# Optimization experiments

Measured on AMD Instinct MI355X. Metric: run time of the kernel, lower is better.

The kernel has to match this reference:

```python
import jax, jax.numpy as jnp
import numpy as np

N, E, F_IN, H = 50000, 800000, 500, 96

def setup_inputs() -> dict:
    key = jax.random.key(0)
    ks = jax.random.split(key, 10)
    x = jax.random.normal(ks[0], (N, F_IN), dtype=jnp.float32)
    src = jax.random.randint(ks[1], (E,), 0, N, dtype=jnp.int32)
    dst = jax.random.randint(ks[2], (E,), 0, N, dtype=jnp.int32)
    perm = jax.random.permutation(ks[3], N).astype(jnp.int32)
    W1 = jax.random.normal(ks[4], (F_IN, H), dtype=jnp.float32) / np.sqrt(F_IN)
    b1 = jnp.zeros((H,), jnp.float32)
    a1 = jnp.full((H,), 0.25, jnp.float32)  # PReLU init
    W2 = jax.random.normal(ks[5], (H, H), dtype=jnp.float32) / np.sqrt(H)
    b2 = jnp.zeros((H,), jnp.float32)
    a2 = jnp.full((H,), 0.25, jnp.float32)
    Wm = jax.random.normal(ks[6], (H, H), dtype=jnp.float32) / np.sqrt(H)
    bm = jnp.zeros((H,), jnp.float32)
    return {"x": x, "src": src, "dst": dst, "perm": perm,
            "W1": W1, "b1": b1, "a1": a1, "W2": W2, "b2": b2, "a2": a2,
            "Wm": Wm, "bm": bm}

def reference(x, src, dst, perm, W1, b1, a1, W2, b2, a2, Wm, bm):
    n = x.shape[0]
    ones = jnp.ones_like(src, dtype=x.dtype)
    deg_out = jnp.clip(jax.ops.segment_sum(ones, src, num_segments=n), 1.0)
    deg_in = jnp.clip(jax.ops.segment_sum(ones, dst, num_segments=n), 1.0)
    norm_out = (deg_out ** -0.5)[:, None]  # [N,1]
    norm_in = (deg_in ** -0.5)[:, None]

    def gconv(h, W, b, a):
        # DGL GraphConv, norm='both': D_out^-1/2 -> W -> A -> D_in^-1/2 -> +b -> PReLU
        h = (h * norm_out) @ W                                  # [N,H]
        agg = jax.ops.segment_sum(h[src], dst, num_segments=n)  # SpMM via gather/scatter
        h = agg * norm_in + b
        return jnp.where(h >= 0, h, a * h)                      # PReLU

    def encode(feat):
        h = gconv(feat, W1, b1, a1)
        return gconv(h, W2, b2, a2)

    z1 = encode(x)
    z2 = encode(x[perm])  # corrupted view: permuted node features
    z1 = z1 @ Wm + bm
    z2 = z2 @ Wm + bm
    return jnp.concatenate([z1.sum(1), z2.sum(1)], axis=0)  # [2N]
```

## Files before the change

kernel.cpp:

```cpp
#include <hip/hip_runtime.h>

#define H96 96

typedef __attribute__((ext_vector_type(8))) short bf16x8_t;
typedef __attribute__((ext_vector_type(4))) float f32x4_t;
typedef __attribute__((ext_vector_type(8))) _Float16 half8_t;

#define NRANGE 8
#define NCHUNK 64

__global__ __launch_bounds__(256) void hist2_kernel(const int* __restrict__ src,
                                                    const int* __restrict__ dst,
                                                    unsigned short* __restrict__ parts,
                                                    int E, int RS, int ecpc) {
    extern __shared__ int h[];
    int r = blockIdx.x >> 6;
    int c = blockIdx.x & 63;
    int lo = r * RS;
    for (int i = threadIdx.x; i < 2 * RS; i += 256) h[i] = 0;
    __syncthreads();
    int e0 = c * ecpc;
    int e1 = min(e0 + ecpc, E);
    for (int base = e0 + threadIdx.x * 4; base < e1; base += 1024) {
        int cnt = min(4, e1 - base);
        if (cnt == 4) {
            int4 sv = *(const int4*)(src + base);
            int4 dv = *(const int4*)(dst + base);
            int a;
            a = sv.x - lo; if ((unsigned)a < (unsigned)RS) atomicAdd(&h[a], 1);
            a = sv.y - lo; if ((unsigned)a < (unsigned)RS) atomicAdd(&h[a], 1);
            a = sv.z - lo; if ((unsigned)a < (unsigned)RS) atomicAdd(&h[a], 1);
            a = sv.w - lo; if ((unsigned)a < (unsigned)RS) atomicAdd(&h[a], 1);
            a = dv.x - lo; if ((unsigned)a < (unsigned)RS) atomicAdd(&h[RS + a], 1);
            a = dv.y - lo; if ((unsigned)a < (unsigned)RS) atomicAdd(&h[RS + a], 1);
            a = dv.z - lo; if ((unsigned)a < (unsigned)RS) atomicAdd(&h[RS + a], 1);
            a = dv.w - lo; if ((unsigned)a < (unsigned)RS) atomicAdd(&h[RS + a], 1);
        } else {
            for (int k = 0; k < cnt; k++) {
                int a = src[base + k] - lo;
                if ((unsigned)a < (unsigned)RS) atomicAdd(&h[a], 1);
                a = dst[base + k] - lo;
                if ((unsigned)a < (unsigned)RS) atomicAdd(&h[RS + a], 1);
            }
        }
    }
    __syncthreads();
    unsigned short* po = parts + ((size_t)(r * 2 + 0) * NCHUNK + c) * RS;
    unsigned short* pi = parts + ((size_t)(r * 2 + 1) * NCHUNK + c) * RS;
    for (int i = threadIdx.x; i < RS; i += 256) {
        po[i] = (unsigned short)h[i];
        pi[i] = (unsigned short)h[RS + i];
    }
}

__global__ void degred_kernel(const unsigned short* __restrict__ parts,
                              const int* __restrict__ perm,
                              int* __restrict__ deg_in, int* __restrict__ iperm,
                              float* __restrict__ no, float* __restrict__ ni,
                              int N, int RS) {
    int i = blockIdx.x * 256 + threadIdx.x;
    if (i >= N) return;
    int r = i / RS, idx = i - r * RS;
    const unsigned short* po = parts + ((size_t)(r * 2 + 0) * NCHUNK) * RS + idx;
    const unsigned short* pi = parts + ((size_t)(r * 2 + 1) * NCHUNK) * RS + idx;
    int so = 0, si = 0;
#pragma unroll
    for (int c = 0; c < NCHUNK; c++) {
        so += po[(size_t)c * RS];
        si += pi[(size_t)c * RS];
    }
    deg_in[i] = si;
    no[i] = rsqrtf(fmaxf((float)so, 1.0f));
    ni[i] = rsqrtf(fmaxf((float)si, 1.0f));
    iperm[perm[i]] = i;
}

__global__ void chunkpre_kernel(const unsigned short* __restrict__ parts,
                                const int* __restrict__ row_start,
                                int* __restrict__ cpre, int N, int RS) {
    int i = blockIdx.x * 256 + threadIdx.x;
    if (i >= N) return;
    int r = i / RS, idx = i - r * RS;
    const unsigned short* pi = parts + ((size_t)(r * 2 + 1) * NCHUNK) * RS + idx;
    int run = row_start[i];
#pragma unroll
    for (int c = 0; c < NCHUNK; c++) {
        cpre[(size_t)c * N + i] = run;
        run += pi[(size_t)c * RS];
    }
}

__global__ void scanA_kernel(const int* __restrict__ in, int* __restrict__ pre,
                             int* __restrict__ bsums, int n) {
    __shared__ int s[256];
    int i = blockIdx.x * 256 + threadIdx.x;
    int v = (i < n) ? in[i] : 0;
    s[threadIdx.x] = v;
    __syncthreads();
    for (int off = 1; off < 256; off <<= 1) {
        int t = (threadIdx.x >= off) ? s[threadIdx.x - off] : 0;
        __syncthreads();
        s[threadIdx.x] += t;
        __syncthreads();
    }
    if (i < n) pre[i] = s[threadIdx.x] - v;
    if (threadIdx.x == 255) bsums[blockIdx.x] = s[255];
}

__global__ void scanB_kernel(int* __restrict__ bsums, int nb) {
    __shared__ int s[256];
    int v = (threadIdx.x < nb) ? bsums[threadIdx.x] : 0;
    s[threadIdx.x] = v;
    __syncthreads();
    for (int off = 1; off < 256; off <<= 1) {
        int t = (threadIdx.x >= off) ? s[threadIdx.x - off] : 0;
        __syncthreads();
        s[threadIdx.x] += t;
        __syncthreads();
    }
    if (threadIdx.x < nb) bsums[threadIdx.x] = s[threadIdx.x] - v;
}

__global__ void rowfin_kernel(const int* __restrict__ pre, const int* __restrict__ bsums,
                              int* __restrict__ row_start, int N, int E) {
    int i = blockIdx.x * 256 + threadIdx.x;
    if (i < N) row_start[i] = pre[i] + bsums[blockIdx.x];
    if (i == 0) row_start[N] = E;
}

__global__ __launch_bounds__(256) void scatter8_kernel(const int* __restrict__ src,
                                                       const int* __restrict__ dst,
                                                       const float* __restrict__ norm_out,
                                                       const int* __restrict__ cpre,
                                                       int2* __restrict__ edge2,
                                                       int E, int N, int RS, int ecpc) {
    extern __shared__ int cur[];
    int r = blockIdx.x >> 6, c = blockIdx.x & 63;
    int lo = r * RS;
    int len = min(RS, N - lo);
    for (int i = threadIdx.x; i < len; i += 256)
        cur[i] = cpre[(size_t)c * N + lo + i];
    __syncthreads();
    int e0 = c * ecpc, e1 = min(e0 + ecpc, E);
    for (int e = e0 + threadIdx.x; e < e1; e += 256) {
        int d = dst[e] - lo;
        if ((unsigned)d < (unsigned)len) {
            int s = src[e];
            int p = atomicAdd(&cur[d], 1);
            edge2[p] = make_int2(s, __float_as_int(norm_out[s]));
        }
    }
}

__global__ void histblk_kernel(const int* __restrict__ deg, int* __restrict__ hb,
                               int N, int nb) {
    __shared__ int h[256];
    h[threadIdx.x] = 0;
    __syncthreads();
    int i = blockIdx.x * 256 + threadIdx.x;
    if (i < N) atomicAdd(&h[min(deg[i], 255)], 1);
    __syncthreads();
    hb[threadIdx.x * nb + blockIdx.x] = h[threadIdx.x];
}

__global__ void place2_kernel(const int* __restrict__ deg, const int* __restrict__ hpre,
                              const int* __restrict__ bsums, int* __restrict__ order,
                              int N, int nb) {
    __shared__ int cur[256];
    int idx = threadIdx.x * nb + blockIdx.x;
    cur[threadIdx.x] = hpre[idx] + bsums[idx >> 8];
    __syncthreads();
    int i = blockIdx.x * 256 + threadIdx.x;
    if (i < N) {
        int b = min(deg[i], 255);
        int p = atomicAdd(&cur[b], 1);
        order[p] = i;
    }
}

__device__ __forceinline__ void f2bf2(float v, unsigned short& h, unsigned short& l) {
    unsigned int b = __float_as_uint(v);
    unsigned short hh = (unsigned short)((b + 0x7FFFu + ((b >> 16) & 1u)) >> 16);
    float fh = __uint_as_float(((unsigned int)hh) << 16);
    float r = v - fh;
    unsigned int rb = __float_as_uint(r);
    unsigned short ll = (unsigned short)((rb + 0x7FFFu + ((rb >> 16) & 1u)) >> 16);
    h = hh; l = ll;
}

__device__ __forceinline__ void cvt8(const float f[8], bf16x8_t& ah, bf16x8_t& al) {
    union { unsigned int u[4]; bf16x8_t v; } H, L;
#pragma unroll
    for (int i = 0; i < 4; i++) {
        float v0 = f[2 * i], v1 = f[2 * i + 1];
        unsigned int b0 = __float_as_uint(v0);
        unsigned int b1 = __float_as_uint(v1);
        unsigned int m0 = b0 & 0xFFFF0000u;
        unsigned int m1 = b1 & 0xFFFF0000u;
        float r0 = v0 - __uint_as_float(m0);
        float r1 = v1 - __uint_as_float(m1);
        H.u[i] = (b0 >> 16) | m1;
        L.u[i] = (__float_as_uint(r0) >> 16) | (__float_as_uint(r1) & 0xFFFF0000u);
    }
    ah = H.v; al = L.v;
}

__global__ void weights_prep(const float* __restrict__ W1, const float* __restrict__ W2,
                             const float* __restrict__ Wm, const float* __restrict__ bm,
                             unsigned short* __restrict__ w1h, unsigned short* __restrict__ w1l,
                             unsigned short* __restrict__ w2h, unsigned short* __restrict__ w2l,
                             float* __restrict__ wsum, float* __restrict__ bsum,
                             int F, int KP1) {
    int idx = blockIdx.x * 256 + threadIdx.x;
    int z1 = 96 * KP1, z2 = z1 + 96 * 96;
    if (idx < z1) {
        int n = idx / KP1, k = idx - n * KP1;
        float v = (k < F) ? W1[(size_t)k * 96 + n] : 0.f;
        unsigned short h, l;
        f2bf2(v, h, l);
        w1h[idx] = h; w1l[idx] = l;
    } else if (idx < z2) {
        int t = idx - z1;
        int n = t / 96, k = t - n * 96;
        float v = W2[(size_t)k * 96 + n];
        unsigned short h, l;
        f2bf2(v, h, l);
        w2h[t] = h; w2l[t] = l;
    } else if (idx < z2 + 96) {
        int c = idx - z2;
        float s = 0.f;
        for (int j = 0; j < 96; j++) s += Wm[c * 96 + j];
        wsum[c] = s;
    } else if (idx == z2 + 96) {
        float s = 0.f;
        for (int j = 0; j < 96; j++) s += bm[j];
        bsum[0] = s;
    }
}

#define GBK 32

__device__ __forceinline__ void gload_lds16(const void* g, void* l) {
    __builtin_amdgcn_global_load_lds(
        (const __attribute__((address_space(1))) unsigned int*)g,
        (__attribute__((address_space(3))) unsigned int*)l, 16, 0, 0);
}

__global__ __launch_bounds__(256, 6) void gemm_mfma(const void* __restrict__ Av,
                                                    const unsigned short* __restrict__ Bth,
                                                    const unsigned short* __restrict__ Btl,
                                                    _Float16* __restrict__ C16,
                                                    const int* __restrict__ ipermArr,
                                                    int M, int K, int KP) {
    __shared__ alignas(16) unsigned short Bs[2][2][96][4][8];
    int tid = threadIdx.x;
    int wid = tid >> 6, lane = tid & 63;
    int q = lane >> 4, mn = lane & 15;
    int rg = wid >> 1, ch = wid & 1;
    int row0 = blockIdx.x * 32 + rg * 16;
    int arow = min(row0 + mn, M - 1);
    int nk = (K + GBK - 1) / GBK;

    const float* A32 = (const float*)Av;

    const unsigned short* gsrc[3];
    int lbase[3];
#pragma unroll
    for (int i = 0; i < 3; i++) {
        int c = wid * 192 + i * 64 + lane;
        int part = (c >= 384) ? 1 : 0;
        int rem = c - part * 384;
        int row = rem >> 2, slot = rem & 3;
        int kc = slot ^ ((row >> 1) & 3);
        gsrc[i] = (part ? Btl : Bth) + (size_t)row * KP + kc * 8;
        lbase[i] = (wid * 192 + i * 64) * 8;
    }

    auto stage = [&](int t, int buf) {
#pragma unroll
        for (int i = 0; i < 3; i++)
            gload_lds16(gsrc[i] + (size_t)t * GBK, &Bs[buf][0][0][0][0] + lbase[i]);
    };

    auto loadA = [&](int t, float* f) {
        int gk = t * GBK + q * 8;
        if (gk + 8 <= K) {
            float4 v0 = *(const float4*)(A32 + (size_t)arow * K + gk);
            float4 v1 = *(const float4*)(A32 + (size_t)arow * K + gk + 4);
            f[0] = v0.x; f[1] = v0.y; f[2] = v0.z; f[3] = v0.w;
            f[4] = v1.x; f[5] = v1.y; f[6] = v1.z; f[7] = v1.w;
        } else {
#pragma unroll
            for (int c = 0; c < 8; c++)
                f[c] = (gk + c < K) ? A32[(size_t)arow * K + gk + c] : 0.f;
        }
    };

    f32x4_t acc[3] = {};
    float f[8], fn[8];

    stage(0, 0);
    loadA(0, f);

    int slotR = q ^ ((mn >> 1) & 3);

    for (int t = 0; t < nk; t++) {
        int tn = (t + 1 < nk) ? t + 1 : nk - 1;
        stage(tn, (t + 1) & 1);
        loadA(tn, fn);
        asm volatile("s_waitcnt vmcnt(5)" ::: "memory");
        __builtin_amdgcn_sched_barrier(0);
        __builtin_amdgcn_s_barrier();

        bf16x8_t ah, al;
        cvt8(f, ah, al);

        const unsigned short* bp = &Bs[t & 1][0][0][0][0] + mn * 32 + slotR * 8 + ch * 1536;
#pragma unroll
        for (int ct2 = 0; ct2 < 3; ct2++) {
            bf16x8_t bh = *(const bf16x8_t*)(bp + ct2 * 512);
            bf16x8_t bl = *(const bf16x8_t*)(bp + 3072 + ct2 * 512);
            acc[ct2] = __builtin_amdgcn_mfma_f32_16x16x32_bf16(ah, bh, acc[ct2], 0, 0, 0);
            acc[ct2] = __builtin_amdgcn_mfma_f32_16x16x32_bf16(ah, bl, acc[ct2], 0, 0, 0);
            acc[ct2] = __builtin_amdgcn_mfma_f32_16x16x32_bf16(al, bh, acc[ct2], 0, 0, 0);
        }
        asm volatile("s_waitcnt lgkmcnt(0)" ::: "memory");
        __builtin_amdgcn_sched_barrier(0);
        __builtin_amdgcn_s_barrier();

#pragma unroll
        for (int c = 0; c < 8; c++) f[c] = fn[c];
    }

    asm volatile("s_waitcnt vmcnt(0)" ::: "memory");
    __builtin_amdgcn_sched_barrier(0);

#pragma unroll
    for (int reg = 0; reg < 4; reg++) {
        int gr = row0 + q * 4 + reg;
        if (gr < M) {
            int ip = ipermArr[gr];
#pragma unroll
            for (int ct2 = 0; ct2 < 3; ct2++) {
                int col = (ch * 3 + ct2) * 16 + mn;
                _Float16 v = (_Float16)acc[ct2][reg];
                C16[(size_t)gr * 192 + col] = v;
                C16[(size_t)ip * 192 + 96 + col] = v;
            }
        }
    }
}

__global__ __launch_bounds__(256, 4) void gemm_small(const _Float16* __restrict__ A16,
                                                     const unsigned short* __restrict__ Bth,
                                                     const unsigned short* __restrict__ Btl,
                                                     _Float16* __restrict__ C16,
                                                     int M) {
    __shared__ alignas(16) unsigned short Bs[3][2][96][4][8];
    const int K = 96;
    int tid = threadIdx.x;
    int wid = tid >> 6, lane = tid & 63;
    int q = lane >> 4, mn = lane & 15;
    int row0 = blockIdx.x * 64 + wid * 16;
    int arow = min(row0 + mn, M - 1);

    const unsigned short* gsrc[3];
    int lbase[3];
#pragma unroll
    for (int i = 0; i < 3; i++) {
        int c = wid * 192 + i * 64 + lane;
        int part = (c >= 384) ? 1 : 0;
        int rem = c - part * 384;
        int row = rem >> 2, slot = rem & 3;
        int kc = slot ^ ((row >> 1) & 3);
        gsrc[i] = (part ? Btl : Bth) + (size_t)row * K + kc * 8;
        lbase[i] = (wid * 192 + i * 64) * 8;
    }

#pragma unroll
    for (int t = 0; t < 3; t++)
#pragma unroll
        for (int i = 0; i < 3; i++)
            gload_lds16(gsrc[i] + (size_t)t * GBK, &Bs[t][0][0][0][0] + lbase[i]);

    uint4 ra0 = *(const uint4*)(A16 + (size_t)arow * K + 0 * GBK + q * 8);
    uint4 ra1 = *(const uint4*)(A16 + (size_t)arow * K + 1 * GBK + q * 8);
    uint4 ra2 = *(const uint4*)(A16 + (size_t)arow * K + 2 * GBK + q * 8);

    asm volatile("s_waitcnt vmcnt(0)" ::: "memory");
    __builtin_amdgcn_sched_barrier(0);
    __builtin_amdgcn_s_barrier();

    f32x4_t acc[6] = {};
    int slotR = q ^ ((mn >> 1) & 3);

    auto step = [&](int t, const uint4& raw) {
        float f[8];
        const _Float16* hp = (const _Float16*)&raw;
#pragma unroll
        for (int c = 0; c < 8; c++) f[c] = (float)hp[c];
        bf16x8_t ah, al;
        cvt8(f, ah, al);
        const unsigned short* bp = &Bs[t][0][0][0][0] + mn * 32 + slotR * 8;
#pragma unroll
        for (int ct = 0; ct < 6; ct++) {
            bf16x8_t bh = *(const bf16x8_t*)(bp + ct * 512);
            bf16x8_t bl = *(const bf16x8_t*)(bp + 3072 + ct * 512);
            acc[ct] = __builtin_amdgcn_mfma_f32_16x16x32_bf16(ah, bh, acc[ct], 0, 0, 0);
            acc[ct] = __builtin_amdgcn_mfma_f32_16x16x32_bf16(ah, bl, acc[ct], 0, 0, 0);
            acc[ct] = __builtin_amdgcn_mfma_f32_16x16x32_bf16(al, bh, acc[ct], 0, 0, 0);
        }
    };

    step(0, ra0);
    step(1, ra1);
    step(2, ra2);

#pragma unroll
    for (int reg = 0; reg < 4; reg++) {
        int gr = row0 + q * 4 + reg;
        if (gr < M) {
#pragma unroll
            for (int ct = 0; ct < 6; ct++)
                C16[(size_t)gr * H96 + ct * 16 + mn] = (_Float16)acc[ct][reg];
        }
    }
}

__device__ __forceinline__ void fmah8(float4& a, float4& b, float s, half8_t v) {
    a.x = fmaf(s, (float)v[0], a.x); a.y = fmaf(s, (float)v[1], a.y);
    a.z = fmaf(s, (float)v[2], a.z); a.w = fmaf(s, (float)v[3], a.w);
    b.x = fmaf(s, (float)v[4], b.x); b.y = fmaf(s, (float)v[5], b.y);
    b.z = fmaf(s, (float)v[6], b.z); b.w = fmaf(s, (float)v[7], b.w);
}

__device__ __forceinline__ float4 prelu4(float4 acc, float ni, float4 b, float4 a) {
    float4 h;
    h.x = fmaf(acc.x, ni, b.x); h.x = (h.x >= 0.f) ? h.x : a.x * h.x;
    h.y = fmaf(acc.y, ni, b.y); h.y = (h.y >= 0.f) ? h.y : a.y * h.y;
    h.z = fmaf(acc.z, ni, b.z); h.z = (h.z >= 0.f) ? h.z : a.z * h.z;
    h.w = fmaf(acc.w, ni, b.w); h.w = (h.w >= 0.f) ? h.w : a.w * h.w;
    return h;
}

__global__ __launch_bounds__(384) void spmm1_dual(
        const half8_t* __restrict__ yp, const int* __restrict__ row_start,
        const int2* __restrict__ edge2, const int* __restrict__ order,
        const float* __restrict__ norm_out, const float* __restrict__ norm_in,
        const float* __restrict__ b1, const float* __restrict__ a1,
        half8_t* __restrict__ hpair, int N) {
    int g = blockIdx.x * 32 + threadIdx.y;
    if (g >= N) return;
    int d = order[g];
    int tx = threadIdx.x;
    int beg = row_start[d], end = row_start[d + 1];
    const half8_t* yt = yp + tx;
    float4 a1a = {0,0,0,0}, a1b = {0,0,0,0}, a2a = {0,0,0,0}, a2b = {0,0,0,0};
    int j = beg;
    for (; j + 8 <= end; j += 8) {
        int2 e[8];
#pragma unroll
        for (int q = 0; q < 8; q++) e[q] = edge2[j + q];
        half8_t u[8], w[8];
#pragma unroll
        for (int q = 0; q < 8; q++) u[q] = yt[(size_t)e[q].x * 24];
#pragma unroll
        for (int q = 0; q < 8; q++) w[q] = yt[(size_t)e[q].x * 24 + 12];
#pragma unroll
        for (int q = 0; q < 8; q++) {
            float n = __int_as_float(e[q].y);
            fmah8(a1a, a1b, n, u[q]);
            fmah8(a2a, a2b, n, w[q]);
        }
    }
    for (; j < end; j++) {
        int2 e = edge2[j];
        float n = __int_as_float(e.y);
        fmah8(a1a, a1b, n, yt[(size_t)e.x * 24]);
        fmah8(a2a, a2b, n, yt[(size_t)e.x * 24 + 12]);
    }
    float ni = norm_in[d], no = norm_out[d];
    float4 bb0 = ((const float4*)b1)[tx * 2], bb1 = ((const float4*)b1)[tx * 2 + 1];
    float4 aa0 = ((const float4*)a1)[tx * 2], aa1 = ((const float4*)a1)[tx * 2 + 1];
    float4 r1a = prelu4(a1a, ni, bb0, aa0), r1b = prelu4(a1b, ni, bb1, aa1);
    float4 r2a = prelu4(a2a, ni, bb0, aa0), r2b = prelu4(a2b, ni, bb1, aa1);
    half8_t o1, o2;
    o1[0] = (_Float16)(r1a.x * no); o1[1] = (_Float16)(r1a.y * no);
    o1[2] = (_Float16)(r1a.z * no); o1[3] = (_Float16)(r1a.w * no);
    o1[4] = (_Float16)(r1b.x * no); o1[5] = (_Float16)(r1b.y * no);
    o1[6] = (_Float16)(r1b.z * no); o1[7] = (_Float16)(r1b.w * no);
    o2[0] = (_Float16)(r2a.x * no); o2[1] = (_Float16)(r2a.y * no);
    o2[2] = (_Float16)(r2a.z * no); o2[3] = (_Float16)(r2a.w * no);
    o2[4] = (_Float16)(r2b.x * no); o2[5] = (_Float16)(r2b.y * no);
    o2[6] = (_Float16)(r2b.z * no); o2[7] = (_Float16)(r2b.w * no);
    hpair[(size_t)d * 24 + tx] = o1;
    hpair[(size_t)d * 24 + 12 + tx] = o2;
}

__global__ __launch_bounds__(384) void spmm2_dual(
        const half8_t* __restrict__ th,
        const int* __restrict__ row_start, const int2* __restrict__ edge2,
        const int* __restrict__ order, const float* __restrict__ norm_in,
        const float* __restrict__ b2, const float* __restrict__ a2,
        const float* __restrict__ wsum, const float* __restrict__ bsum,
        float* __restrict__ outp, int N) {
    int g = blockIdx.x * 32 + threadIdx.y;
    int tx = threadIdx.x;
    int ty = threadIdx.y;
    bool valid = (g < N);
    int d = valid ? order[g] : 0;
    int beg = 0, end = 0;
    if (valid) { beg = row_start[d]; end = row_start[d + 1]; }
    const half8_t* t1 = th + tx;
    float4 a1a = {0,0,0,0}, a1b = {0,0,0,0}, a2a = {0,0,0,0}, a2b = {0,0,0,0};
    int j = beg;
    for (; j + 8 <= end; j += 8) {
        int s[8];
#pragma unroll
        for (int q = 0; q < 8; q++) s[q] = edge2[j + q].x;
        half8_t u[8], w[8];
#pragma unroll
        for (int q = 0; q < 8; q++) u[q] = t1[(size_t)s[q] * 24];
#pragma unroll
        for (int q = 0; q < 8; q++) w[q] = t1[(size_t)s[q] * 24 + 12];
#pragma unroll
        for (int q = 0; q < 8; q++) {
            fmah8(a1a, a1b, 1.f, u[q]);
            fmah8(a2a, a2b, 1.f, w[q]);
        }
    }
    for (; j < end; j++) {
        int s = edge2[j].x;
        fmah8(a1a, a1b, 1.f, t1[(size_t)s * 24]);
        fmah8(a2a, a2b, 1.f, t1[(size_t)s * 24 + 12]);
    }
    float ni = valid ? norm_in[d] : 0.f;
    float4 bb0 = ((const float4*)b2)[tx * 2], bb1 = ((const float4*)b2)[tx * 2 + 1];
    float4 aa0 = ((const float4*)a2)[tx * 2], aa1 = ((const float4*)a2)[tx * 2 + 1];
    float4 wv0 = ((const float4*)wsum)[tx * 2], wv1 = ((const float4*)wsum)[tx * 2 + 1];
    float4 r1a = prelu4(a1a, ni, bb0, aa0), r1b = prelu4(a1b, ni, bb1, aa1);
    float4 r2a = prelu4(a2a, ni, bb0, aa0), r2b = prelu4(a2b, ni, bb1, aa1);
    float p1 = r1a.x * wv0.x + r1a.y * wv0.y + r1a.z * wv0.z + r1a.w * wv0.w
             + r1b.x * wv1.x + r1b.y * wv1.y + r1b.z * wv1.z + r1b.w * wv1.w;
    float p2 = r2a.x * wv0.x + r2a.y * wv0.y + r2a.z * wv0.z + r2a.w * wv0.w
             + r2b.x * wv1.x + r2b.y * wv1.y + r2b.z * wv1.z + r2b.w * wv1.w;
    __shared__ float red1[32][12];
    __shared__ float red2[32][12];
    red1[ty][tx] = p1;
    red2[ty][tx] = p2;
    __syncthreads();
    if (tx == 0 && valid) {
        float s1 = 0.f, s2 = 0.f;
#pragma unroll
        for (int k = 0; k < 12; k++) { s1 += red1[ty][k]; s2 += red2[ty][k]; }
        outp[d] = s1 + bsum[0];
        outp[N + d] = s2 + bsum[0];
    }
}

extern "C" void kernel_launch(void* const* d_in, const int* in_sizes, int n_in,
                              void* d_out, int out_size, void* d_ws, size_t ws_size,
                              hipStream_t stream) {
    const float* x    = (const float*)d_in[0];
    const int*   src  = (const int*)d_in[1];
    const int*   dst  = (const int*)d_in[2];
    const int*   perm = (const int*)d_in[3];
    const float* W1   = (const float*)d_in[4];
    const float* b1   = (const float*)d_in[5];
    const float* a1   = (const float*)d_in[6];
    const float* W2   = (const float*)d_in[7];
    const float* b2   = (const float*)d_in[8];
    const float* a2   = (const float*)d_in[9];
    const float* Wm   = (const float*)d_in[10];
    const float* bm   = (const float*)d_in[11];
    float* out = (float*)d_out;

    int E = in_sizes[1];
    int N = in_sizes[3];
    int F = in_sizes[0] / N;
    int KP1 = ((F + GBK - 1) / GBK) * GBK;

    size_t NP = ((size_t)N + 256) & ~(size_t)255;
    size_t EP = ((size_t)E + 255) & ~(size_t)255;
    int nb = (N + 255) / 256;
    size_t HB = ((size_t)256 * nb + 255) & ~(size_t)255;

    int* iperm     = (int*)d_ws;
    int* deg_in    = iperm + NP;
    int* pre       = deg_in + NP;
    int* row_start = pre + NP;
    int* cursor    = row_start + NP;
    int* order     = cursor + NP;
    int* bsums     = order + NP;
    int* hb        = bsums + 256;
    int* hpre      = hb + HB;
    int2* edge2    = (int2*)(hpre + HB);
    float* norm_out = (float*)(edge2 + EP);
    float* norm_in  = norm_out + NP;
    float* wsum     = norm_in + NP;
    float* bsum     = wsum + 128;
    unsigned short* w1th = (unsigned short*)(bsum + 128);
    unsigned short* w1tl = w1th + 49664;
    unsigned short* w2th = w1tl + 49664;
    unsigned short* w2tl = w2th + 9728;
    _Float16* fpA = (_Float16*)(w2tl + 9728);
    _Float16* fpB = fpA + ((size_t)N * 192 + 256);
    _Float16* ypair = fpA;
    _Float16* hpair = fpB;
    _Float16* th    = fpA;

    unsigned short* parts = (unsigned short*)fpA;
    int* cpre = (int*)fpB;

    int RS = (N + NRANGE - 1) / NRANGE;
    int ecpc = ((E + NCHUNK - 1) / NCHUNK + 3) & ~3;
    hist2_kernel<<<NRANGE * NCHUNK, 256, 2 * RS * (int)sizeof(int), stream>>>(
        src, dst, parts, E, RS, ecpc);
    degred_kernel<<<(N + 255) / 256, 256, 0, stream>>>(parts, perm, deg_in, iperm,
                                                       norm_out, norm_in, N, RS);

    scanA_kernel<<<nb, 256, 0, stream>>>(deg_in, pre, bsums, N);
    scanB_kernel<<<1, 256, 0, stream>>>(bsums, nb);
    rowfin_kernel<<<nb, 256, 0, stream>>>(pre, bsums, row_start, N, E);
    chunkpre_kernel<<<(N + 255) / 256, 256, 0, stream>>>(parts, row_start, cpre, N, RS);
    scatter8_kernel<<<NRANGE * NCHUNK, 256, RS * (int)sizeof(int), stream>>>(
        src, dst, norm_out, cpre, edge2, E, N, RS, ecpc);

    histblk_kernel<<<nb, 256, 0, stream>>>(deg_in, hb, N, nb);
    int n2 = 256 * nb;
    int nb2 = (n2 + 255) / 256;
    scanA_kernel<<<nb2, 256, 0, stream>>>(hb, hpre, bsums, n2);
    scanB_kernel<<<1, 256, 0, stream>>>(bsums, nb2);
    place2_kernel<<<nb, 256, 0, stream>>>(deg_in, hpre, bsums, order, N, nb);

    int wtot = 96 * KP1 + 96 * 96 + 96 + 1;
    weights_prep<<<(wtot + 255) / 256, 256, 0, stream>>>(W1, W2, Wm, bm, w1th, w1tl,
                                                         w2th, w2tl, wsum, bsum, F, KP1);

    gemm_mfma<<<(N + 31) / 32, 256, 0, stream>>>(x, w1th, w1tl, ypair, iperm,
                                                 N, F, KP1);

    int nsb = (N + 31) / 32;
    spmm1_dual<<<nsb, dim3(12, 32), 0, stream>>>(
        (const half8_t*)ypair, row_start, edge2, order, norm_out, norm_in,
        b1, a1, (half8_t*)hpair, N);

    gemm_small<<<(2 * N + 63) / 64, 256, 0, stream>>>(hpair, w2th, w2tl, th, 2 * N);

    spmm2_dual<<<nsb, dim3(12, 32), 0, stream>>>(
        (const half8_t*)th, row_start, edge2, order, norm_in, b2, a2,
        wsum, bsum, out, N);
}
```

Before: 405.0 us.

## Give each wave all 96 columns and prefetch A two tiles ahead in gemm_mfma

Each block now covers 64 rows instead of 32, and each wave computes a 16x96 tile (6 accumulators) instead of 16x48. That halves the number of blocks and the B tile staging per row, so each LDS-staged B tile is reused by twice as many rows. The A-row loads are now double buffered two K-steps ahead by alternating f0/f1 buffers, which removes the register copy and gives loads more time to land. The cost is more accumulator and A registers per wave at launch_bounds(256,6), which may cause spills or lower occupancy, plus half as many blocks across the CUs.

```diff
diff --git a/kernel.cpp b/kernel.cpp
--- a/kernel.cpp
+++ b/kernel.cpp
@@ -256,8 +256,7 @@
     int tid = threadIdx.x;
     int wid = tid >> 6, lane = tid & 63;
     int q = lane >> 4, mn = lane & 15;
-    int rg = wid >> 1, ch = wid & 1;
-    int row0 = blockIdx.x * 32 + rg * 16;
+    int row0 = blockIdx.x * 64 + wid * 16;
     int arow = min(row0 + mn, M - 1);
     int nk = (K + GBK - 1) / GBK;
 
@@ -296,40 +295,43 @@
         }
     };
 
-    f32x4_t acc[3] = {};
-    float f[8], fn[8];
-
-    stage(0, 0);
-    loadA(0, f);
-
+    f32x4_t acc[6] = {};
     int slotR = q ^ ((mn >> 1) & 3);
 
-    for (int t = 0; t < nk; t++) {
-        int tn = (t + 1 < nk) ? t + 1 : nk - 1;
-        stage(tn, (t + 1) & 1);
-        loadA(tn, fn);
+    auto body = [&](int t, float (&cur)[8]) {
+        int tn1 = (t + 1 < nk) ? t + 1 : nk - 1;
+        stage(tn1, (t + 1) & 1);
         asm volatile("s_waitcnt vmcnt(5)" ::: "memory");
         __builtin_amdgcn_sched_barrier(0);
         __builtin_amdgcn_s_barrier();
 
         bf16x8_t ah, al;
-        cvt8(f, ah, al);
-
-        const unsigned short* bp = &Bs[t & 1][0][0][0][0] + mn * 32 + slotR * 8 + ch * 1536;
-#pragma unroll
-        for (int ct2 = 0; ct2 < 3; ct2++) {
-            bf16x8_t bh = *(const bf16x8_t*)(bp + ct2 * 512);
-            bf16x8_t bl = *(const bf16x8_t*)(bp + 3072 + ct2 * 512);
-            acc[ct2] = __builtin_amdgcn_mfma_f32_16x16x32_bf16(ah, bh, acc[ct2], 0, 0, 0);
-            acc[ct2] = __builtin_amdgcn_mfma_f32_16x16x32_bf16(ah, bl, acc[ct2], 0, 0, 0);
-            acc[ct2] = __builtin_amdgcn_mfma_f32_16x16x32_bf16(al, bh, acc[ct2], 0, 0, 0);
+        cvt8(cur, ah, al);
+        int tn2 = (t + 2 < nk) ? t + 2 : nk - 1;
+        loadA(tn2, cur);
+
+        const unsigned short* bp = &Bs[t & 1][0][0][0][0] + mn * 32 + slotR * 8;
+#pragma unroll
+        for (int ct = 0; ct < 6; ct++) {
+            bf16x8_t bh = *(const bf16x8_t*)(bp + ct * 512);
+            bf16x8_t bl = *(const bf16x8_t*)(bp + 3072 + ct * 512);
+            acc[ct] = __builtin_amdgcn_mfma_f32_16x16x32_bf16(ah, bh, acc[ct], 0, 0, 0);
+            acc[ct] = __builtin_amdgcn_mfma_f32_16x16x32_bf16(ah, bl, acc[ct], 0, 0, 0);
+            acc[ct] = __builtin_amdgcn_mfma_f32_16x16x32_bf16(al, bh, acc[ct], 0, 0, 0);
         }
         asm volatile("s_waitcnt lgkmcnt(0)" ::: "memory");
         __builtin_amdgcn_sched_barrier(0);
         __builtin_amdgcn_s_barrier();
-
-#pragma unroll
-        for (int c = 0; c < 8; c++) f[c] = fn[c];
+    };
+
+    float f0[8], f1[8];
+    stage(0, 0);
+    loadA(0, f0);
+    loadA(1, f1);
+
+    for (int t0 = 0; t0 < nk; t0 += 2) {
+        body(t0, f0);
+        if (t0 + 1 < nk) body(t0 + 1, f1);
     }
 
     asm volatile("s_waitcnt vmcnt(0)" ::: "memory");
@@ -341,11 +343,10 @@
         if (gr < M) {
             int ip = ipermArr[gr];
 #pragma unroll
-            for (int ct2 = 0; ct2 < 3; ct2++) {
-                int col = (ch * 3 + ct2) * 16 + mn;
-                _Float16 v = (_Float16)acc[ct2][reg];
-                C16[(size_t)gr * 192 + col] = v;
-                C16[(size_t)ip * 192 + 96 + col] = v;
+            for (int ct = 0; ct < 6; ct++) {
+                _Float16 v = (_Float16)acc[ct][reg];
+                C16[(size_t)gr * 192 + ct * 16 + mn] = v;
+                C16[(size_t)ip * 192 + 96 + ct * 16 + mn] = v;
             }
         }
     }
@@ -637,7 +638,7 @@
     weights_prep<<<(wtot + 255) / 256, 256, 0, stream>>>(W1, W2, Wm, bm, w1th, w1tl,
                                                          w2th, w2tl, wsum, bsum, F, KP1);
 
-    gemm_mfma<<<(N + 31) / 32, 256, 0, stream>>>(x, w1th, w1tl, ypair, iperm,
+    gemm_mfma<<<(N + 63) / 64, 256, 0, stream>>>(x, w1th, w1tl, ypair, iperm,
                                                  N, F, KP1);
 
     int nsb = (N + 31) / 32;
```

Measured after the change: 389.9 us. -3.7%, faster.
